# Kernel tuning notes

Measured on AMD Instinct MI355X. Metric: run time of the kernel, lower is better.

The kernel has to match this reference:

```python
import jax, jax.numpy as jnp
import numpy as np

N_STATE = 5
N_CONTROL = 5
NEURONS = 1024
BATCH = 131072
IN_DIM = 3 * N_STATE + 2 * N_CONTROL  # 25


def setup_inputs() -> dict:
    key = jax.random.key(0)
    ks = jax.random.split(key, 11)

    def w(k, shape, fan_in):
        return jax.random.normal(k, shape, jnp.float32) / np.sqrt(fan_in).astype(np.float32)

    return {
        "x": jax.random.normal(ks[0], (BATCH, IN_DIM), jnp.float32),
        "Wx": w(ks[1], (2, N_STATE), N_STATE),
        "bx": jnp.zeros((2,), jnp.float32),
        "Wu": w(ks[2], (2, N_CONTROL), N_CONTROL),
        "bu": jnp.zeros((2,), jnp.float32),
        "W1": w(ks[3], (NEURONS, 10), 10),
        "b1": jnp.zeros((NEURONS,), jnp.float32),
        "W2": w(ks[4], (NEURONS, NEURONS), NEURONS),
        "b2": jnp.zeros((NEURONS,), jnp.float32),
        "W3": w(ks[5], (3, NEURONS), NEURONS),
        "b3": jnp.zeros((3,), jnp.float32),
    }


def reference(x, Wx, bx, Wu, bu, W1, b1, W2, b2, W3, b3):
    ns = Wx.shape[1]
    # strided gathers over the interleaved state/control layout (vectorized over batch)
    vx_ = x[:, 0:3 * ns:3]          # [B, n_state]
    vy_ = x[:, 1:3 * ns:3]
    r_ = x[:, 2:3 * ns:3]
    th_ = x[:, 3 * ns::2]           # [B, n_control]
    st_ = x[:, 3 * ns + 1::2]

    fx = lambda v: jax.nn.relu(v @ Wx.T + bx)  # [B, 2]
    fu = lambda v: jax.nn.relu(v @ Wu.T + bu)  # [B, 2]

    l1 = jnp.concatenate([fx(vx_), fx(vy_), fx(r_), fu(th_), fu(st_)], axis=-1)  # [B, 10]
    l1 = l1[:, None, :]  # unsqueeze(1) -> [B, 1, 10]

    h = jax.nn.relu(l1 @ W1.T + b1)   # [B, 1, neurons]
    h = jax.nn.relu(h @ W2.T + b2)    # [B, 1, neurons]
    return jax.nn.sigmoid(h @ W3.T + b3)  # [B, 1, 3]
```

## Files before the change

### kernel.cpp

```cpp
#include <hip/hip_runtime.h>
#include <stdint.h>

#define NEUR 1024
#define BM 128
#define BN 512
#define THREADS 512
#define H1S 1040
#define L1S 80

typedef short  s16x8  __attribute__((ext_vector_type(8)));
typedef __bf16 bf16x8 __attribute__((ext_vector_type(8)));
typedef float  f32x16 __attribute__((ext_vector_type(16)));

__device__ __forceinline__ unsigned short f2bf(float f){
  unsigned u = __builtin_bit_cast(unsigned, f);
  u += 0x7FFFu + ((u >> 16) & 1u);
  return (unsigned short)(u >> 16);
}
__device__ __forceinline__ float bf2f(unsigned short h){
  unsigned u = ((unsigned)h) << 16;
  return __builtin_bit_cast(float, u);
}
__device__ __forceinline__ f32x16 mfma32(bf16x8 a, bf16x8 b, f32x16 c){
  return __builtin_amdgcn_mfma_f32_32x32x16_bf16(a, b, c, 0, 0, 0);
}
__device__ __forceinline__ f32x16 zero16(){
  f32x16 v;
#pragma unroll
  for (int r = 0; r < 16; ++r) v[r] = 0.f;
  return v;
}
__device__ __forceinline__ bf16x8 ld16(const void* p){
  return __builtin_bit_cast(bf16x8, *reinterpret_cast<const s16x8*>(p));
}

__global__ void prep_kernel(const float* __restrict__ W1, const float* __restrict__ W2,
                            unsigned short* __restrict__ w2opt, unsigned short* __restrict__ w1opt){
  const int nchunks = NEUR * 128;
  const int total = nchunks + 4096;
  for (int i = blockIdx.x*blockDim.x + threadIdx.x; i < total; i += gridDim.x*blockDim.x){
    if (i < nchunks){
      const int col = i >> 7, c8 = i & 127;
      const float* src = W2 + (size_t)col*NEUR + c8*8;
      const int ks = c8 >> 1, lf = c8 & 1, lane = lf*32 + (col & 31), nt = col >> 5;
      unsigned short* dst = w2opt + (((size_t)(nt*64 + ks)*64 + lane) * 8);
#pragma unroll
      for (int j = 0; j < 8; ++j) dst[j] = f2bf(src[j]);
    } else {
      const int o = i - nchunks;
      const int nt = o >> 7, ks = (o >> 6) & 1, lane = o & 63;
      const int col = nt*32 + (lane & 31);
      unsigned short* dst = w1opt + (size_t)o * 8;
#pragma unroll
      for (int j = 0; j < 8; ++j){
        const int k = ks*16 + (lane >> 5)*8 + j;
        dst[j] = (k < 10) ? f2bf(W1[col*10 + k]) : (unsigned short)0;
      }
    }
  }
}

__global__ void finish_kernel(const float* __restrict__ pws, const float* __restrict__ b3,
                              float* __restrict__ out, int batch){
  const int total = batch * 3;
  for (int i = blockIdx.x*blockDim.x + threadIdx.x; i < total; i += gridDim.x*blockDim.x){
    const int j = i - (i/3)*3;
    const float v = pws[i] + pws[(size_t)total + i] + b3[j];
    out[i] = 1.f / (1.f + __expf(-v));
  }
}

__global__ __launch_bounds__(THREADS, 2) void mlp_kernel(
    const float* __restrict__ x,
    const float* __restrict__ Wx, const float* __restrict__ bxp,
    const float* __restrict__ Wu, const float* __restrict__ bup,
    const float* __restrict__ b1, const float* __restrict__ b2,
    const float* __restrict__ W3,
    const unsigned short* __restrict__ w2opt, const unsigned short* __restrict__ w1opt,
    float* __restrict__ pws, int batch)
{
  extern __shared__ char smem[];
  char* l1p = smem;
  char* h1  = smem + BM*L1S;

  const int tid = threadIdx.x;
  const int l   = tid & 63;
  const int wid = tid >> 6;
  const int l31 = l & 31;
  const int lh  = l >> 5;
  const int wm  = wid >> 2;
  const int wn  = wid & 3;
  const int bm  = blockIdx.x >> 1;
  const int bn  = blockIdx.x & 1;
  const long rbase = (long)bm * BM;

  float* xs = (float*)h1;
  for (int i = tid; i < BM*25; i += THREADS) xs[i] = x[rbase*25 + i];
  __syncthreads();

  if (tid < BM){
    const float* xr = xs + tid*25;
    float l1v[10];
#pragma unroll
    for (int g = 0; g < 3; ++g)
#pragma unroll
      for (int o = 0; o < 2; ++o){
        float s = bxp[o];
#pragma unroll
        for (int i = 0; i < 5; ++i) s += xr[g + 3*i] * Wx[o*5 + i];
        l1v[g*2 + o] = fmaxf(s, 0.f);
      }
#pragma unroll
    for (int g = 0; g < 2; ++g)
#pragma unroll
      for (int o = 0; o < 2; ++o){
        float s = bup[o];
#pragma unroll
        for (int i = 0; i < 5; ++i) s += xr[15 + g + 2*i] * Wu[o*5 + i];
        l1v[6 + g*2 + o] = fmaxf(s, 0.f);
      }
    unsigned short* dst = (unsigned short*)(l1p + tid*L1S);
#pragma unroll
    for (int i = 0; i < 10; ++i) dst[i] = f2bf(l1v[i]);
#pragma unroll
    for (int i = 10; i < 32; ++i) dst[i] = 0;
  }
  __syncthreads();

  f32x16 acc[2][4];
#pragma unroll
  for (int mt = 0; mt < 2; ++mt)
#pragma unroll
    for (int nt = 0; nt < 4; ++nt) acc[mt][nt] = zero16();

  const int aBase = (wm*64 + l31)*H1S + lh*16;

  for (int h = 0; h < 2; ++h){
#pragma unroll
    for (int st = 0; st < 2; ++st){
      f32x16 c00 = zero16(), c01 = zero16(), c10 = zero16(), c11 = zero16();
      const int colh = st*256 + wn*64;
      const int ntg  = h*16 + st*8 + wn*2;
#pragma unroll
      for (int ks = 0; ks < 2; ++ks){
        bf16x8 a0 = ld16(l1p + (wm*64 + l31)*L1S + ks*32 + lh*16);
        bf16x8 a1 = ld16(l1p + (wm*64 + 32 + l31)*L1S + ks*32 + lh*16);
        bf16x8 b0 = ld16(w1opt + (((size_t)(ntg + 0)*2 + ks)*64 + l) * 8);
        bf16x8 b1f= ld16(w1opt + (((size_t)(ntg + 1)*2 + ks)*64 + l) * 8);
        c00 = mfma32(a0, b0, c00);
        c10 = mfma32(a1, b0, c10);
        c01 = mfma32(a0, b1f, c01);
        c11 = mfma32(a1, b1f, c11);
      }
#pragma unroll
      for (int nt2 = 0; nt2 < 2; ++nt2){
        const int colHalf = colh + nt2*32 + l31;
        const float bv = b1[h*512 + colHalf];
        const f32x16& cA = nt2 ? c01 : c00;
        const f32x16& cB = nt2 ? c11 : c10;
#pragma unroll
        for (int r = 0; r < 16; ++r){
          const int rr = (r & 3) + 8*(r >> 2) + 4*lh;
          *reinterpret_cast<unsigned short*>(h1 + (wm*64 + rr)*H1S + colHalf*2) =
              f2bf(fmaxf(cA[r] + bv, 0.f));
          *reinterpret_cast<unsigned short*>(h1 + (wm*64 + 32 + rr)*H1S + colHalf*2) =
              f2bf(fmaxf(cB[r] + bv, 0.f));
        }
      }
    }
    __syncthreads();

    {
      const size_t hoff = (size_t)h * 32768;
      const char* pb0 = (const char*)w2opt + (((size_t)(bn*16 + wn*4 + 0)*64)*64 + l)*16 + hoff;
      const char* pb1 = (const char*)w2opt + (((size_t)(bn*16 + wn*4 + 1)*64)*64 + l)*16 + hoff;
      const char* pb2 = (const char*)w2opt + (((size_t)(bn*16 + wn*4 + 2)*64)*64 + l)*16 + hoff;
      const char* pb3 = (const char*)w2opt + (((size_t)(bn*16 + wn*4 + 3)*64)*64 + l)*16 + hoff;
      int ao = aBase;

      bf16x8 Aa0, Aa1, Ab0, Ab1;
      bf16x8 P0a, P0b, Q0a, Q0b, P1a, P1b, Q1a, Q1b;

#define MM4_01(A0_,A1_,B0_,B1_) do{ __builtin_amdgcn_s_setprio(1);            \
      acc[0][0]=mfma32(A0_,B0_,acc[0][0]); acc[1][0]=mfma32(A1_,B0_,acc[1][0]);\
      acc[0][1]=mfma32(A0_,B1_,acc[0][1]); acc[1][1]=mfma32(A1_,B1_,acc[1][1]);\
      __builtin_amdgcn_s_setprio(0); }while(0)
#define MM4_23(A0_,A1_,B0_,B1_) do{ __builtin_amdgcn_s_setprio(1);            \
      acc[0][2]=mfma32(A0_,B0_,acc[0][2]); acc[1][2]=mfma32(A1_,B0_,acc[1][2]);\
      acc[0][3]=mfma32(A0_,B1_,acc[0][3]); acc[1][3]=mfma32(A1_,B1_,acc[1][3]);\
      __builtin_amdgcn_s_setprio(0); }while(0)

      P0a = ld16(pb0);          P0b = ld16(pb1);
      Q0a = ld16(pb2);          Q0b = ld16(pb3);
      P1a = ld16(pb0 + 1024);   P1b = ld16(pb1 + 1024);
      Aa0 = ld16(h1 + ao);      Aa1 = ld16(h1 + ao + 32*H1S);

      for (int t = 0; t < 15; ++t){
        Q1a = ld16(pb2 + 1024);  Q1b = ld16(pb3 + 1024);
        Ab0 = ld16(h1 + ao + 32); Ab1 = ld16(h1 + ao + 32*H1S + 32);
        MM4_01(Aa0, Aa1, P0a, P0b);
        P0a = ld16(pb0 + 2048);  P0b = ld16(pb1 + 2048);
        MM4_23(Aa0, Aa1, Q0a, Q0b);
        Q0a = ld16(pb2 + 2048);  Q0b = ld16(pb3 + 2048);
        Aa0 = ld16(h1 + ao + 64); Aa1 = ld16(h1 + ao + 32*H1S + 64);
        MM4_01(Ab0, Ab1, P1a, P1b);
        P1a = ld16(pb0 + 3072);  P1b = ld16(pb1 + 3072);
        MM4_23(Ab0, Ab1, Q1a, Q1b);
        pb0 += 2048; pb1 += 2048; pb2 += 2048; pb3 += 2048; ao += 64;
      }
      Q1a = ld16(pb2 + 1024);  Q1b = ld16(pb3 + 1024);
      Ab0 = ld16(h1 + ao + 32); Ab1 = ld16(h1 + ao + 32*H1S + 32);
      MM4_01(Aa0, Aa1, P0a, P0b);
      MM4_23(Aa0, Aa1, Q0a, Q0b);
      MM4_01(Ab0, Ab1, P1a, P1b);
      MM4_23(Ab0, Ab1, Q1a, Q1b);
#undef MM4_01
#undef MM4_23
    }
    __syncthreads();
  }

  float* sp = (float*)l1p;
  {
    float b2v[4], w30[4], w31[4], w32[4];
#pragma unroll
    for (int nt = 0; nt < 4; ++nt){
      const int colg = bn*512 + wn*128 + nt*32 + l31;
      b2v[nt] = b2[colg];
      w30[nt] = W3[0*NEUR + colg];
      w31[nt] = W3[1*NEUR + colg];
      w32[nt] = W3[2*NEUR + colg];
    }
#pragma unroll
    for (int mf = 0; mf < 2; ++mf){
      float p0[16], p1[16], p2[16];
#pragma unroll
      for (int r = 0; r < 16; ++r){ p0[r] = 0.f; p1[r] = 0.f; p2[r] = 0.f; }
#pragma unroll
      for (int nt = 0; nt < 4; ++nt)
#pragma unroll
        for (int r = 0; r < 16; ++r){
          const float hv = fmaxf(acc[mf][nt][r] + b2v[nt], 0.f);
          p0[r] += hv * w30[nt];
          p1[r] += hv * w31[nt];
          p2[r] += hv * w32[nt];
        }
#pragma unroll
      for (int off = 1; off < 32; off <<= 1)
#pragma unroll
        for (int r = 0; r < 16; ++r){
          p0[r] += __shfl_xor(p0[r], off, 64);
          p1[r] += __shfl_xor(p1[r], off, 64);
          p2[r] += __shfl_xor(p2[r], off, 64);
        }
      if (l31 == 0){
#pragma unroll
        for (int r = 0; r < 16; ++r){
          const int row = wm*64 + mf*32 + (r & 3) + 8*(r >> 2) + 4*lh;
          float* d = sp + ((size_t)wn*BM + row)*3;
          d[0] = p0[r]; d[1] = p1[r]; d[2] = p2[r];
        }
      }
    }
  }
  __syncthreads();

  for (int t2 = tid; t2 < BM*3; t2 += THREADS){
    const int row = t2 / 3, j = t2 - row*3;
    const float v = sp[(0*BM + row)*3 + j] + sp[(1*BM + row)*3 + j]
                  + sp[(2*BM + row)*3 + j] + sp[(3*BM + row)*3 + j];
    pws[((size_t)bn*batch + rbase + row)*3 + j] = v;
  }
}

__global__ __launch_bounds__(THREADS, 2) void mlp_kernel_old(
    const float* __restrict__ x,
    const float* __restrict__ Wx, const float* __restrict__ bxp,
    const float* __restrict__ Wu, const float* __restrict__ bup,
    const float* __restrict__ W1, const float* __restrict__ b1,
    const float* __restrict__ W2f, const float* __restrict__ b2,
    const float* __restrict__ W3, const float* __restrict__ b3,
    float* __restrict__ out)
{
  extern __shared__ char smem[];
  unsigned short* l1p = (unsigned short*)smem;
  char* h1 = smem + 5120;
  const int tid = threadIdx.x, l = tid & 63, wid = tid >> 6;
  const int l31 = l & 31, lh = l >> 5;
  const long rbase = (long)blockIdx.x * 64;

  float* xs = (float*)h1;
  for (int i = tid; i < 64*25; i += THREADS) xs[i] = x[rbase*25 + i];
  __syncthreads();
  if (tid < 64){
    const float* xr = xs + tid*25;
    float l1v[10];
#pragma unroll
    for (int g = 0; g < 3; ++g)
#pragma unroll
      for (int o = 0; o < 2; ++o){
        float s = bxp[o];
#pragma unroll
        for (int i = 0; i < 5; ++i) s += xr[g + 3*i] * Wx[o*5 + i];
        l1v[g*2 + o] = fmaxf(s, 0.f);
      }
#pragma unroll
    for (int g = 0; g < 2; ++g)
#pragma unroll
      for (int o = 0; o < 2; ++o){
        float s = bup[o];
#pragma unroll
        for (int i = 0; i < 5; ++i) s += xr[15 + g + 2*i] * Wu[o*5 + i];
        l1v[6 + g*2 + o] = fmaxf(s, 0.f);
      }
    unsigned short* dst = l1p + tid*40;
#pragma unroll
    for (int i = 0; i < 10; ++i) dst[i] = f2bf(l1v[i]);
#pragma unroll
    for (int i = 10; i < 32; ++i) dst[i] = 0;
  }
  __syncthreads();

  f32x16 c[2][4];
#pragma unroll
  for (int mt = 0; mt < 2; ++mt)
#pragma unroll
    for (int nt = 0; nt < 4; ++nt) c[mt][nt] = zero16();
#pragma unroll
  for (int ks = 0; ks < 2; ++ks){
    bf16x8 a0 = ld16(smem + l31*80 + ks*32 + lh*16);
    bf16x8 a1 = ld16(smem + (32 + l31)*80 + ks*32 + lh*16);
#pragma unroll
    for (int nt = 0; nt < 4; ++nt){
      const int col = wid*128 + nt*32 + l31;
      s16x8 raw;
#pragma unroll
      for (int j = 0; j < 8; ++j){
        const int k = ks*16 + lh*8 + j;
        raw[j] = (k < 10) ? (short)f2bf(W1[col*10 + k]) : (short)0;
      }
      bf16x8 b = __builtin_bit_cast(bf16x8, raw);
      c[0][nt] = mfma32(a0, b, c[0][nt]);
      c[1][nt] = mfma32(a1, b, c[1][nt]);
    }
  }
#pragma unroll
  for (int nt = 0; nt < 4; ++nt){
    const int col = wid*128 + nt*32 + l31;
    const float bv = b1[col];
#pragma unroll
    for (int mt = 0; mt < 2; ++mt)
#pragma unroll
      for (int r = 0; r < 16; ++r){
        const int row = mt*32 + (r & 3) + 8*(r >> 2) + 4*lh;
        *reinterpret_cast<unsigned short*>(h1 + row*2064 + col*2) =
            f2bf(fmaxf(c[mt][nt][r] + bv, 0.f));
      }
  }
  __syncthreads();

  f32x16 acc[2][4];
#pragma unroll
  for (int mt = 0; mt < 2; ++mt)
#pragma unroll
    for (int nt = 0; nt < 4; ++nt) acc[mt][nt] = zero16();
  const int aA0 = l31*2064 + lh*16;
  for (int ks = 0; ks < 64; ++ks){
    bf16x8 A0 = ld16(h1 + aA0 + ks*32);
    bf16x8 A1 = ld16(h1 + aA0 + 32*2064 + ks*32);
#pragma unroll
    for (int nt = 0; nt < 4; ++nt){
      const int col = wid*128 + nt*32 + l31;
      const float* p = W2f + (size_t)col*NEUR + ks*16 + lh*8;
      s16x8 raw;
#pragma unroll
      for (int j = 0; j < 8; ++j) raw[j] = (short)f2bf(p[j]);
      bf16x8 B = __builtin_bit_cast(bf16x8, raw);
      acc[0][nt] = mfma32(A0, B, acc[0][nt]);
      acc[1][nt] = mfma32(A1, B, acc[1][nt]);
    }
  }
  __syncthreads();
#pragma unroll
  for (int nt = 0; nt < 4; ++nt){
    const int col = wid*128 + nt*32 + l31;
    const float bv = b2[col];
#pragma unroll
    for (int mt = 0; mt < 2; ++mt)
#pragma unroll
      for (int r = 0; r < 16; ++r){
        const int row = mt*32 + (r & 3) + 8*(r >> 2) + 4*lh;
        *reinterpret_cast<unsigned short*>(h1 + row*2064 + col*2) =
            f2bf(fmaxf(acc[mt][nt][r] + bv, 0.f));
      }
  }
  __syncthreads();
  float s[8][3];
#pragma unroll
  for (int rr = 0; rr < 8; ++rr)
#pragma unroll
    for (int j = 0; j < 3; ++j) s[rr][j] = 0.f;
#pragma unroll
  for (int h = 0; h < 2; ++h){
    const int k0 = h*512 + l*8;
    float w3v[3][8];
#pragma unroll
    for (int j = 0; j < 3; ++j)
#pragma unroll
      for (int i = 0; i < 8; ++i) w3v[j][i] = W3[j*NEUR + k0 + i];
#pragma unroll
    for (int rr = 0; rr < 8; ++rr){
      const int row = wid*8 + rr;
      s16x8 raw = *reinterpret_cast<const s16x8*>(h1 + row*2064 + k0*2);
#pragma unroll
      for (int i = 0; i < 8; ++i){
        const float hv = bf2f((unsigned short)raw[i]);
        s[rr][0] += hv * w3v[0][i];
        s[rr][1] += hv * w3v[1][i];
        s[rr][2] += hv * w3v[2][i];
      }
    }
  }
#pragma unroll
  for (int off = 1; off < 64; off <<= 1)
#pragma unroll
    for (int rr = 0; rr < 8; ++rr)
#pragma unroll
      for (int j = 0; j < 3; ++j) s[rr][j] += __shfl_xor(s[rr][j], off, 64);
  if (l == 0){
#pragma unroll
    for (int rr = 0; rr < 8; ++rr){
      const int row = wid*8 + rr;
#pragma unroll
      for (int j = 0; j < 3; ++j)
        out[(rbase + row)*3 + j] = 1.f / (1.f + __expf(-(s[rr][j] + b3[j])));
    }
  }
}

extern "C" void kernel_launch(void* const* d_in, const int* in_sizes, int n_in,
                              void* d_out, int out_size, void* d_ws, size_t ws_size,
                              hipStream_t stream){
  const float* x  = (const float*)d_in[0];
  const float* Wx = (const float*)d_in[1];
  const float* bx = (const float*)d_in[2];
  const float* Wu = (const float*)d_in[3];
  const float* bu = (const float*)d_in[4];
  const float* W1 = (const float*)d_in[5];
  const float* b1 = (const float*)d_in[6];
  const float* W2 = (const float*)d_in[7];
  const float* b2 = (const float*)d_in[8];
  const float* W3 = (const float*)d_in[9];
  const float* b3 = (const float*)d_in[10];
  float* out = (float*)d_out;

  const int batch = in_sizes[0] / 25;
  const size_t w2_bytes  = (size_t)NEUR*NEUR*2;
  const size_t w1_bytes  = (size_t)4096*8*2;
  const size_t pws_bytes = (size_t)batch*3*2*4;
  const size_t ws_need   = w2_bytes + w1_bytes + pws_bytes;

  if (ws_size >= ws_need && (batch % BM) == 0){
    unsigned short* w2opt = (unsigned short*)d_ws;
    unsigned short* w1opt = (unsigned short*)((char*)d_ws + w2_bytes);
    float* pws            = (float*)((char*)d_ws + w2_bytes + w1_bytes);

    prep_kernel<<<512, 256, 0, stream>>>(W1, W2, w2opt, w1opt);

    const int smem = BM*L1S + BM*H1S;
    hipFuncSetAttribute(reinterpret_cast<const void*>(mlp_kernel),
                        hipFuncAttributeMaxDynamicSharedMemorySize, smem);
    const int nblocks = (batch / BM) * 2;
    mlp_kernel<<<nblocks, THREADS, smem, stream>>>(
        x, Wx, bx, Wu, bu, b1, b2, W3, w2opt, w1opt, pws, batch);

    finish_kernel<<<(batch*3 + 255)/256, 256, 0, stream>>>(pws, b3, out, batch);
  } else {
    const int smem = 5120 + 64*2064;
    hipFuncSetAttribute(reinterpret_cast<const void*>(mlp_kernel_old),
                        hipFuncAttributeMaxDynamicSharedMemorySize, smem);
    mlp_kernel_old<<<batch/64, THREADS, smem, stream>>>(
        x, Wx, bx, Wu, bu, W1, b1, W2, b2, W3, b3, out);
  }
}
```

Measured before the change: 363.7 us.

## Stage W2 tiles into LDS via async global_load_lds double buffering

The W2 operand is now copied from global memory into a double-buffered LDS staging area with global_load_lds, where before each wave loaded it straight into registers. The K loop is split into four quarters, each computing 256 columns of the first layer into a smaller h1 buffer, and the second-layer K dimension is walked in 32-wide chunks with a barrier after each chunk. The aim is to share W2 loads across the two M-warps and overlap the global fetch with MFMA work. In exchange there are many more __syncthreads calls, and LDS use grows to about 141KB per block, which may cut occupancy below the 2 blocks per CU requested in launch bounds.

```diff
diff --git a/kernel.cpp b/kernel.cpp
--- a/kernel.cpp
+++ b/kernel.cpp
@@ -3,9 +3,8 @@
 
 #define NEUR 1024
 #define BM 128
-#define BN 512
 #define THREADS 512
-#define H1S 1040
+#define H1S 528
 #define L1S 80
 
 typedef short  s16x8  __attribute__((ext_vector_type(8)));
@@ -32,6 +31,11 @@
 }
 __device__ __forceinline__ bf16x8 ld16(const void* p){
   return __builtin_bit_cast(bf16x8, *reinterpret_cast<const s16x8*>(p));
+}
+__device__ __forceinline__ void gll16(const void* gsrc, void* ldst){
+  __builtin_amdgcn_global_load_lds(
+      (const __attribute__((address_space(1))) unsigned int*)gsrc,
+      (__attribute__((address_space(3))) unsigned int*)ldst, 16, 0, 0);
 }
 
 __global__ void prep_kernel(const float* __restrict__ W1, const float* __restrict__ W2,
@@ -82,6 +86,8 @@
   extern __shared__ char smem[];
   char* l1p = smem;
   char* h1  = smem + BM*L1S;
+  char* bb0 = h1 + BM*H1S;
+  char* bb1 = bb0 + 32768;
 
   const int tid = threadIdx.x;
   const int l   = tid & 63;
@@ -133,20 +139,56 @@
 #pragma unroll
     for (int nt = 0; nt < 4; ++nt) acc[mt][nt] = zero16();
 
-  const int aBase = (wm*64 + l31)*H1S + lh*16;
-
-  for (int h = 0; h < 2; ++h){
-#pragma unroll
-    for (int st = 0; st < 2; ++st){
+  const int a0off = (wm*64 + l31)*H1S + lh*16;
+  const int a1off = a0off + 32*H1S;
+  const int bro0  = ((wn*4 + 0)*2)*1024 + l*16;
+  const int bro1  = ((wn*4 + 1)*2)*1024 + l*16;
+  const int bro2  = ((wn*4 + 2)*2)*1024 + l*16;
+  const int bro3  = ((wn*4 + 3)*2)*1024 + l*16;
+
+#define STAGE(G, DST) do{                                                         \
+    const char* s_ = (const char*)w2opt +                                         \
+        (((size_t)(bn*16 + wid*2)*64 + 2*(G))*64 + l)*16;                         \
+    char* d_ = (DST) + wid*4096;                                                  \
+    gll16(s_,                 d_);                                                \
+    gll16(s_ + 1024,          d_ + 1024);                                         \
+    gll16(s_ + 65536,         d_ + 2048);                                         \
+    gll16(s_ + 65536 + 1024,  d_ + 3072);                                         \
+  }while(0)
+
+#define CHUNK(C, CUR, DO_STAGE, NXT, GNEXT) do{                                   \
+    if (DO_STAGE) STAGE(GNEXT, NXT);                                              \
+    _Pragma("unroll")                                                             \
+    for (int ksl = 0; ksl < 2; ++ksl){                                            \
+      const int kq_ = (C)*2 + ksl;                                                \
+      bf16x8 A0 = ld16(h1 + a0off + kq_*32);                                      \
+      bf16x8 A1 = ld16(h1 + a1off + kq_*32);                                      \
+      bf16x8 B0 = ld16((CUR) + bro0 + ksl*1024);                                  \
+      bf16x8 B1 = ld16((CUR) + bro1 + ksl*1024);                                  \
+      bf16x8 B2 = ld16((CUR) + bro2 + ksl*1024);                                  \
+      bf16x8 B3 = ld16((CUR) + bro3 + ksl*1024);                                  \
+      __builtin_amdgcn_s_setprio(1);                                              \
+      acc[0][0]=mfma32(A0,B0,acc[0][0]); acc[1][0]=mfma32(A1,B0,acc[1][0]);       \
+      acc[0][1]=mfma32(A0,B1,acc[0][1]); acc[1][1]=mfma32(A1,B1,acc[1][1]);       \
+      acc[0][2]=mfma32(A0,B2,acc[0][2]); acc[1][2]=mfma32(A1,B2,acc[1][2]);       \
+      acc[0][3]=mfma32(A0,B3,acc[0][3]); acc[1][3]=mfma32(A1,B3,acc[1][3]);       \
+      __builtin_amdgcn_s_setprio(0);                                              \
+    }                                                                             \
+    __syncthreads();                                                              \
+  }while(0)
+
+  STAGE(0, bb0);
+
+  for (int q = 0; q < 4; ++q){
+    {
       f32x16 c00 = zero16(), c01 = zero16(), c10 = zero16(), c11 = zero16();
-      const int colh = st*256 + wn*64;
-      const int ntg  = h*16 + st*8 + wn*2;
 #pragma unroll
       for (int ks = 0; ks < 2; ++ks){
         bf16x8 a0 = ld16(l1p + (wm*64 + l31)*L1S + ks*32 + lh*16);
         bf16x8 a1 = ld16(l1p + (wm*64 + 32 + l31)*L1S + ks*32 + lh*16);
-        bf16x8 b0 = ld16(w1opt + (((size_t)(ntg + 0)*2 + ks)*64 + l) * 8);
-        bf16x8 b1f= ld16(w1opt + (((size_t)(ntg + 1)*2 + ks)*64 + l) * 8);
+        const int ntg = q*8 + wn*2;
+        bf16x8 b0 = ld16(w1opt + (((size_t)(ntg + 0)*2 + ks)*64 + l)*8);
+        bf16x8 b1f= ld16(w1opt + (((size_t)(ntg + 1)*2 + ks)*64 + l)*8);
         c00 = mfma32(a0, b0, c00);
         c10 = mfma32(a1, b0, c10);
         c01 = mfma32(a0, b1f, c01);
@@ -154,71 +196,32 @@
       }
 #pragma unroll
       for (int nt2 = 0; nt2 < 2; ++nt2){
-        const int colHalf = colh + nt2*32 + l31;
-        const float bv = b1[h*512 + colHalf];
+        const int colq = wn*64 + nt2*32 + l31;
+        const float bv = b1[q*256 + colq];
         const f32x16& cA = nt2 ? c01 : c00;
         const f32x16& cB = nt2 ? c11 : c10;
 #pragma unroll
         for (int r = 0; r < 16; ++r){
           const int rr = (r & 3) + 8*(r >> 2) + 4*lh;
-          *reinterpret_cast<unsigned short*>(h1 + (wm*64 + rr)*H1S + colHalf*2) =
-              f2bf(fmaxf(cA[r] + bv, 0.f));
-          *reinterpret_cast<unsigned short*>(h1 + (wm*64 + 32 + rr)*H1S + colHalf*2) =
-              f2bf(fmaxf(cB[r] + bv, 0.f));
+          *(unsigned short*)(h1 + (wm*64 + rr)*H1S + colq*2)      = f2bf(fmaxf(cA[r] + bv, 0.f));
+          *(unsigned short*)(h1 + (wm*64 + 32 + rr)*H1S + colq*2) = f2bf(fmaxf(cB[r] + bv, 0.f));
         }
       }
     }
     __syncthreads();
 
-    {
-      const size_t hoff = (size_t)h * 32768;
-      const char* pb0 = (const char*)w2opt + (((size_t)(bn*16 + wn*4 + 0)*64)*64 + l)*16 + hoff;
-      const char* pb1 = (const char*)w2opt + (((size_t)(bn*16 + wn*4 + 1)*64)*64 + l)*16 + hoff;
-      const char* pb2 = (const char*)w2opt + (((size_t)(bn*16 + wn*4 + 2)*64)*64 + l)*16 + hoff;
-      const char* pb3 = (const char*)w2opt + (((size_t)(bn*16 + wn*4 + 3)*64)*64 + l)*16 + hoff;
-      int ao = aBase;
-
-      bf16x8 Aa0, Aa1, Ab0, Ab1;
-      bf16x8 P0a, P0b, Q0a, Q0b, P1a, P1b, Q1a, Q1b;
-
-#define MM4_01(A0_,A1_,B0_,B1_) do{ __builtin_amdgcn_s_setprio(1);            \
-      acc[0][0]=mfma32(A0_,B0_,acc[0][0]); acc[1][0]=mfma32(A1_,B0_,acc[1][0]);\
-      acc[0][1]=mfma32(A0_,B1_,acc[0][1]); acc[1][1]=mfma32(A1_,B1_,acc[1][1]);\
-      __builtin_amdgcn_s_setprio(0); }while(0)
-#define MM4_23(A0_,A1_,B0_,B1_) do{ __builtin_amdgcn_s_setprio(1);            \
-      acc[0][2]=mfma32(A0_,B0_,acc[0][2]); acc[1][2]=mfma32(A1_,B0_,acc[1][2]);\
-      acc[0][3]=mfma32(A0_,B1_,acc[0][3]); acc[1][3]=mfma32(A1_,B1_,acc[1][3]);\
-      __builtin_amdgcn_s_setprio(0); }while(0)
-
-      P0a = ld16(pb0);          P0b = ld16(pb1);
-      Q0a = ld16(pb2);          Q0b = ld16(pb3);
-      P1a = ld16(pb0 + 1024);   P1b = ld16(pb1 + 1024);
-      Aa0 = ld16(h1 + ao);      Aa1 = ld16(h1 + ao + 32*H1S);
-
-      for (int t = 0; t < 15; ++t){
-        Q1a = ld16(pb2 + 1024);  Q1b = ld16(pb3 + 1024);
-        Ab0 = ld16(h1 + ao + 32); Ab1 = ld16(h1 + ao + 32*H1S + 32);
-        MM4_01(Aa0, Aa1, P0a, P0b);
-        P0a = ld16(pb0 + 2048);  P0b = ld16(pb1 + 2048);
-        MM4_23(Aa0, Aa1, Q0a, Q0b);
-        Q0a = ld16(pb2 + 2048);  Q0b = ld16(pb3 + 2048);
-        Aa0 = ld16(h1 + ao + 64); Aa1 = ld16(h1 + ao + 32*H1S + 64);
-        MM4_01(Ab0, Ab1, P1a, P1b);
-        P1a = ld16(pb0 + 3072);  P1b = ld16(pb1 + 3072);
-        MM4_23(Ab0, Ab1, Q1a, Q1b);
-        pb0 += 2048; pb1 += 2048; pb2 += 2048; pb3 += 2048; ao += 64;
-      }
-      Q1a = ld16(pb2 + 1024);  Q1b = ld16(pb3 + 1024);
-      Ab0 = ld16(h1 + ao + 32); Ab1 = ld16(h1 + ao + 32*H1S + 32);
-      MM4_01(Aa0, Aa1, P0a, P0b);
-      MM4_23(Aa0, Aa1, Q0a, Q0b);
-      MM4_01(Ab0, Ab1, P1a, P1b);
-      MM4_23(Ab0, Ab1, Q1a, Q1b);
-#undef MM4_01
-#undef MM4_23
-    }
-    __syncthreads();
-  }
+    const int g0 = q*8;
+    CHUNK(0, bb0, true,   bb1, g0 + 1);
+    CHUNK(1, bb1, true,   bb0, g0 + 2);
+    CHUNK(2, bb0, true,   bb1, g0 + 3);
+    CHUNK(3, bb1, true,   bb0, g0 + 4);
+    CHUNK(4, bb0, true,   bb1, g0 + 5);
+    CHUNK(5, bb1, true,   bb0, g0 + 6);
+    CHUNK(6, bb0, true,   bb1, g0 + 7);
+    CHUNK(7, bb1, (q < 3), bb0, g0 + 8);
+  }
+#undef STAGE
+#undef CHUNK
 
   float* sp = (float*)l1p;
   {
@@ -467,7 +470,7 @@
 
     prep_kernel<<<512, 256, 0, stream>>>(W1, W2, w2opt, w1opt);
 
-    const int smem = BM*L1S + BM*H1S;
+    const int smem = BM*L1S + BM*H1S + 2*32768;
     hipFuncSetAttribute(reinterpret_cast<const void*>(mlp_kernel),
                         hipFuncAttributeMaxDynamicSharedMemorySize, smem);
     const int nblocks = (batch / BM) * 2;
```

Measured after the change: 371.5 us. +2.1%, slower.

## Chunk layer-1 into K quarters and retile layer-2 warps across all rows

Applied to the files above, without the earlier changes.

Layer-1 activations are now produced in four 256-column chunks. Each chunk is consumed immediately by a layer-2 K-slice, which roughly halves the h1 shared-memory buffer (row stride 1040 to 528 bytes) and should allow better occupancy. Each of the 8 warps now covers all 128 rows and a 64-column slice, instead of a 2x4 warp grid, so every B fragment feeds eight MFMAs but more A loads come from LDS. The final reduction sums partials from 8 warps through a dedicated shared buffer. The cost is four extra barriers per block and more LDS A traffic.

```diff
diff --git a/kernel.cpp b/kernel.cpp
--- a/kernel.cpp
+++ b/kernel.cpp
@@ -3,9 +3,8 @@
 
 #define NEUR 1024
 #define BM 128
-#define BN 512
 #define THREADS 512
-#define H1S 1040
+#define H1S 528
 #define L1S 80
 
 typedef short  s16x8  __attribute__((ext_vector_type(8)));
@@ -82,14 +81,13 @@
   extern __shared__ char smem[];
   char* l1p = smem;
   char* h1  = smem + BM*L1S;
+  float* sp = (float*)(h1 + BM*H1S);
 
   const int tid = threadIdx.x;
   const int l   = tid & 63;
   const int wid = tid >> 6;
   const int l31 = l & 31;
   const int lh  = l >> 5;
-  const int wm  = wid >> 2;
-  const int wn  = wid & 3;
   const int bm  = blockIdx.x >> 1;
   const int bn  = blockIdx.x & 1;
   const long rbase = (long)bm * BM;
@@ -127,120 +125,108 @@
   }
   __syncthreads();
 
-  f32x16 acc[2][4];
-#pragma unroll
-  for (int mt = 0; mt < 2; ++mt)
-#pragma unroll
-    for (int nt = 0; nt < 4; ++nt) acc[mt][nt] = zero16();
-
-  const int aBase = (wm*64 + l31)*H1S + lh*16;
-
-  for (int h = 0; h < 2; ++h){
-#pragma unroll
-    for (int st = 0; st < 2; ++st){
-      f32x16 c00 = zero16(), c01 = zero16(), c10 = zero16(), c11 = zero16();
-      const int colh = st*256 + wn*64;
-      const int ntg  = h*16 + st*8 + wn*2;
+  f32x16 acc[4][2];
+#pragma unroll
+  for (int mt = 0; mt < 4; ++mt)
+#pragma unroll
+    for (int nt = 0; nt < 2; ++nt) acc[mt][nt] = zero16();
+
+  const int a0o = (0*32 + l31)*H1S + lh*16;
+  const int a1o = (1*32 + l31)*H1S + lh*16;
+  const int a2o = (2*32 + l31)*H1S + lh*16;
+  const int a3o = (3*32 + l31)*H1S + lh*16;
+
+#define LDBP(B0_,B1_,B2_,B3_, OFF) do{                       \
+    B0_ = ld16(pb0 + (OFF));        B1_ = ld16(pb1 + (OFF)); \
+    B2_ = ld16(pb0 + (OFF) + 1024); B3_ = ld16(pb1 + (OFF) + 1024); }while(0)
+#define LDA4(A0_,A1_,A2_,A3_, OFF) do{                       \
+    A0_ = ld16(h1 + a0o + (OFF)); A1_ = ld16(h1 + a1o + (OFF)); \
+    A2_ = ld16(h1 + a2o + (OFF)); A3_ = ld16(h1 + a3o + (OFF)); }while(0)
+#define MM8(A0_,A1_,A2_,A3_, Bn0_,Bn1_) do{ __builtin_amdgcn_s_setprio(1); \
+    acc[0][0]=mfma32(A0_,Bn0_,acc[0][0]); acc[0][1]=mfma32(A0_,Bn1_,acc[0][1]); \
+    acc[1][0]=mfma32(A1_,Bn0_,acc[1][0]); acc[1][1]=mfma32(A1_,Bn1_,acc[1][1]); \
+    acc[2][0]=mfma32(A2_,Bn0_,acc[2][0]); acc[2][1]=mfma32(A2_,Bn1_,acc[2][1]); \
+    acc[3][0]=mfma32(A3_,Bn0_,acc[3][0]); acc[3][1]=mfma32(A3_,Bn1_,acc[3][1]); \
+    __builtin_amdgcn_s_setprio(0); }while(0)
+
+  const char* const wB = (const char*)w2opt + ((size_t)(bn*16 + wid*2))*65536 + (size_t)l*16;
+
+  for (int q = 0; q < 4; ++q){
+    const char* pb0 = wB + q*16384;
+    const char* pb1 = pb0 + 65536;
+
+    bf16x8 B00,B01,B02,B03, B10,B11,B12,B13;
+    bf16x8 Aa0,Aa1,Aa2,Aa3, Ab0,Ab1,Ab2,Ab3;
+
+    LDBP(B00,B01,B02,B03, 0);
+
+    {
+      f32x16 c4[4];
+#pragma unroll
+      for (int mt = 0; mt < 4; ++mt) c4[mt] = zero16();
 #pragma unroll
       for (int ks = 0; ks < 2; ++ks){
-        bf16x8 a0 = ld16(l1p + (wm*64 + l31)*L1S + ks*32 + lh*16);
-        bf16x8 a1 = ld16(l1p + (wm*64 + 32 + l31)*L1S + ks*32 + lh*16);
-        bf16x8 b0 = ld16(w1opt + (((size_t)(ntg + 0)*2 + ks)*64 + l) * 8);
-        bf16x8 b1f= ld16(w1opt + (((size_t)(ntg + 1)*2 + ks)*64 + l) * 8);
-        c00 = mfma32(a0, b0, c00);
-        c10 = mfma32(a1, b0, c10);
-        c01 = mfma32(a0, b1f, c01);
-        c11 = mfma32(a1, b1f, c11);
-      }
-#pragma unroll
-      for (int nt2 = 0; nt2 < 2; ++nt2){
-        const int colHalf = colh + nt2*32 + l31;
-        const float bv = b1[h*512 + colHalf];
-        const f32x16& cA = nt2 ? c01 : c00;
-        const f32x16& cB = nt2 ? c11 : c10;
+        bf16x8 bw = ld16(w1opt + (((size_t)(q*8 + wid)*2 + ks)*64 + l)*8);
+#pragma unroll
+        for (int mt = 0; mt < 4; ++mt){
+          bf16x8 aw = ld16(l1p + (mt*32 + l31)*L1S + ks*32 + lh*16);
+          c4[mt] = mfma32(aw, bw, c4[mt]);
+        }
+      }
+      const int colq = wid*32 + l31;
+      const float bv = b1[q*256 + colq];
+#pragma unroll
+      for (int mt = 0; mt < 4; ++mt)
 #pragma unroll
         for (int r = 0; r < 16; ++r){
-          const int rr = (r & 3) + 8*(r >> 2) + 4*lh;
-          *reinterpret_cast<unsigned short*>(h1 + (wm*64 + rr)*H1S + colHalf*2) =
-              f2bf(fmaxf(cA[r] + bv, 0.f));
-          *reinterpret_cast<unsigned short*>(h1 + (wm*64 + 32 + rr)*H1S + colHalf*2) =
-              f2bf(fmaxf(cB[r] + bv, 0.f));
+          const int row = mt*32 + (r & 3) + 8*(r >> 2) + 4*lh;
+          *(unsigned short*)(h1 + row*H1S + colq*2) = f2bf(fmaxf(c4[mt][r] + bv, 0.f));
         }
-      }
     }
     __syncthreads();
 
-    {
-      const size_t hoff = (size_t)h * 32768;
-      const char* pb0 = (const char*)w2opt + (((size_t)(bn*16 + wn*4 + 0)*64)*64 + l)*16 + hoff;
-      const char* pb1 = (const char*)w2opt + (((size_t)(bn*16 + wn*4 + 1)*64)*64 + l)*16 + hoff;
-      const char* pb2 = (const char*)w2opt + (((size_t)(bn*16 + wn*4 + 2)*64)*64 + l)*16 + hoff;
-      const char* pb3 = (const char*)w2opt + (((size_t)(bn*16 + wn*4 + 3)*64)*64 + l)*16 + hoff;
-      int ao = aBase;
-
-      bf16x8 Aa0, Aa1, Ab0, Ab1;
-      bf16x8 P0a, P0b, Q0a, Q0b, P1a, P1b, Q1a, Q1b;
-
-#define MM4_01(A0_,A1_,B0_,B1_) do{ __builtin_amdgcn_s_setprio(1);            \
-      acc[0][0]=mfma32(A0_,B0_,acc[0][0]); acc[1][0]=mfma32(A1_,B0_,acc[1][0]);\
-      acc[0][1]=mfma32(A0_,B1_,acc[0][1]); acc[1][1]=mfma32(A1_,B1_,acc[1][1]);\
-      __builtin_amdgcn_s_setprio(0); }while(0)
-#define MM4_23(A0_,A1_,B0_,B1_) do{ __builtin_amdgcn_s_setprio(1);            \
-      acc[0][2]=mfma32(A0_,B0_,acc[0][2]); acc[1][2]=mfma32(A1_,B0_,acc[1][2]);\
-      acc[0][3]=mfma32(A0_,B1_,acc[0][3]); acc[1][3]=mfma32(A1_,B1_,acc[1][3]);\
-      __builtin_amdgcn_s_setprio(0); }while(0)
-
-      P0a = ld16(pb0);          P0b = ld16(pb1);
-      Q0a = ld16(pb2);          Q0b = ld16(pb3);
-      P1a = ld16(pb0 + 1024);   P1b = ld16(pb1 + 1024);
-      Aa0 = ld16(h1 + ao);      Aa1 = ld16(h1 + ao + 32*H1S);
-
-      for (int t = 0; t < 15; ++t){
-        Q1a = ld16(pb2 + 1024);  Q1b = ld16(pb3 + 1024);
-        Ab0 = ld16(h1 + ao + 32); Ab1 = ld16(h1 + ao + 32*H1S + 32);
-        MM4_01(Aa0, Aa1, P0a, P0b);
-        P0a = ld16(pb0 + 2048);  P0b = ld16(pb1 + 2048);
-        MM4_23(Aa0, Aa1, Q0a, Q0b);
-        Q0a = ld16(pb2 + 2048);  Q0b = ld16(pb3 + 2048);
-        Aa0 = ld16(h1 + ao + 64); Aa1 = ld16(h1 + ao + 32*H1S + 64);
-        MM4_01(Ab0, Ab1, P1a, P1b);
-        P1a = ld16(pb0 + 3072);  P1b = ld16(pb1 + 3072);
-        MM4_23(Ab0, Ab1, Q1a, Q1b);
-        pb0 += 2048; pb1 += 2048; pb2 += 2048; pb3 += 2048; ao += 64;
-      }
-      Q1a = ld16(pb2 + 1024);  Q1b = ld16(pb3 + 1024);
-      Ab0 = ld16(h1 + ao + 32); Ab1 = ld16(h1 + ao + 32*H1S + 32);
-      MM4_01(Aa0, Aa1, P0a, P0b);
-      MM4_23(Aa0, Aa1, Q0a, Q0b);
-      MM4_01(Ab0, Ab1, P1a, P1b);
-      MM4_23(Ab0, Ab1, Q1a, Q1b);
-#undef MM4_01
-#undef MM4_23
+    LDA4(Aa0,Aa1,Aa2,Aa3, 0);
+#pragma unroll
+    for (int t = 0; t < 4; ++t){
+      const int kb = t*4096;
+      const int ka = t*128;
+      LDBP(B10,B11,B12,B13, kb + 2048);
+      LDA4(Ab0,Ab1,Ab2,Ab3, ka + 32);
+      MM8(Aa0,Aa1,Aa2,Aa3, B00,B01);
+      LDA4(Aa0,Aa1,Aa2,Aa3, ka + 64);
+      MM8(Ab0,Ab1,Ab2,Ab3, B02,B03);
+      if (t < 3) LDBP(B00,B01,B02,B03, kb + 4096);
+      LDA4(Ab0,Ab1,Ab2,Ab3, ka + 96);
+      MM8(Aa0,Aa1,Aa2,Aa3, B10,B11);
+      if (t < 3) LDA4(Aa0,Aa1,Aa2,Aa3, ka + 128);
+      MM8(Ab0,Ab1,Ab2,Ab3, B12,B13);
     }
     __syncthreads();
   }
-
-  float* sp = (float*)l1p;
+#undef LDBP
+#undef LDA4
+#undef MM8
+
   {
-    float b2v[4], w30[4], w31[4], w32[4];
-#pragma unroll
-    for (int nt = 0; nt < 4; ++nt){
-      const int colg = bn*512 + wn*128 + nt*32 + l31;
+    float b2v[2], w30[2], w31[2], w32[2];
+#pragma unroll
+    for (int nt = 0; nt < 2; ++nt){
+      const int colg = bn*512 + wid*64 + nt*32 + l31;
       b2v[nt] = b2[colg];
       w30[nt] = W3[0*NEUR + colg];
       w31[nt] = W3[1*NEUR + colg];
       w32[nt] = W3[2*NEUR + colg];
     }
 #pragma unroll
-    for (int mf = 0; mf < 2; ++mf){
+    for (int mt = 0; mt < 4; ++mt){
       float p0[16], p1[16], p2[16];
 #pragma unroll
       for (int r = 0; r < 16; ++r){ p0[r] = 0.f; p1[r] = 0.f; p2[r] = 0.f; }
 #pragma unroll
-      for (int nt = 0; nt < 4; ++nt)
+      for (int nt = 0; nt < 2; ++nt)
 #pragma unroll
         for (int r = 0; r < 16; ++r){
-          const float hv = fmaxf(acc[mf][nt][r] + b2v[nt], 0.f);
+          const float hv = fmaxf(acc[mt][nt][r] + b2v[nt], 0.f);
           p0[r] += hv * w30[nt];
           p1[r] += hv * w31[nt];
           p2[r] += hv * w32[nt];
@@ -256,8 +242,8 @@
       if (l31 == 0){
 #pragma unroll
         for (int r = 0; r < 16; ++r){
-          const int row = wm*64 + mf*32 + (r & 3) + 8*(r >> 2) + 4*lh;
-          float* d = sp + ((size_t)wn*BM + row)*3;
+          const int row = mt*32 + (r & 3) + 8*(r >> 2) + 4*lh;
+          float* d = sp + ((size_t)wid*BM + row)*3;
           d[0] = p0[r]; d[1] = p1[r]; d[2] = p2[r];
         }
       }
@@ -267,8 +253,9 @@
 
   for (int t2 = tid; t2 < BM*3; t2 += THREADS){
     const int row = t2 / 3, j = t2 - row*3;
-    const float v = sp[(0*BM + row)*3 + j] + sp[(1*BM + row)*3 + j]
-                  + sp[(2*BM + row)*3 + j] + sp[(3*BM + row)*3 + j];
+    float v = 0.f;
+#pragma unroll
+    for (int w = 0; w < 8; ++w) v += sp[((size_t)w*BM + row)*3 + j];
     pws[((size_t)bn*batch + rbase + row)*3 + j] = v;
   }
 }
@@ -467,7 +454,7 @@
 
     prep_kernel<<<512, 256, 0, stream>>>(W1, W2, w2opt, w1opt);
 
-    const int smem = BM*L1S + BM*H1S;
+    const int smem = BM*L1S + BM*H1S + 8*BM*3*4;
     hipFuncSetAttribute(reinterpret_cast<const void*>(mlp_kernel),
                         hipFuncAttributeMaxDynamicSharedMemorySize, smem);
     const int nblocks = (batch / BM) * 2;
```

After: 418.7 us. 15.1% more time.
